# Optimization experiments

Hardware: AMD Instinct MI355X
Metric: run time of the kernel (lower is better)

## Reference

```python
import jax, jax.numpy as jnp
import numpy as np

C = 256          # hidden_size
H = 8            # num_heads
HD = C // H      # head dim = 32
W = 8            # window side; N = W*W = 64 tokens per window
N = W * W
NW = 64          # windows per image
B = 32           # images
B_ = B * NW      # 2048


def make_rel_index():
    # identical to the torch buffer construction (meshgrid 'ij')
    coords = np.stack(np.meshgrid(np.arange(W), np.arange(W), indexing='ij'))  # (2,W,W)
    flat = coords.reshape(2, -1)                       # (2, N)
    rel = flat[:, :, None] - flat[:, None, :]          # (2, N, N)
    rel = rel.transpose(1, 2, 0).astype(np.int64)      # (N, N, 2)
    rel[..., 0] += W - 1
    rel[..., 1] += W - 1
    rel[..., 0] *= 2 * W - 1
    return jnp.asarray(rel.sum(-1), jnp.int32)         # (N, N) in [0, 225)


def setup_inputs() -> dict:
    key = jax.random.key(0)
    ks = jax.random.split(key, 12)
    x = jax.random.normal(ks[0], (B_, N, C), jnp.float32)
    # Swin-style additive mask: 0 for allowed, -1e9 for masked pairs
    keep = jax.random.uniform(ks[1], (NW, N, N)) > 0.1
    mask = jnp.where(keep, 0.0, -1e9).astype(jnp.float32)
    std = 0.02
    wq = jax.random.normal(ks[2], (C, C), jnp.float32) * std
    bq = jnp.zeros((C,), jnp.float32)
    wk = jax.random.normal(ks[3], (C, C), jnp.float32) * std
    bk = jnp.zeros((C,), jnp.float32)
    wv = jax.random.normal(ks[4], (C, C), jnp.float32) * std
    bv = jnp.zeros((C,), jnp.float32)
    wp = jax.random.normal(ks[5], (C, C), jnp.float32) * std
    bp = jnp.zeros((C,), jnp.float32)
    bias_table = jax.random.normal(ks[6], ((2 * W - 1) ** 2, H), jnp.float32) * std
    rel_index = make_rel_index()
    return {"x": x, "mask": mask, "wq": wq, "bq": bq, "wk": wk, "bk": bk,
            "wv": wv, "bv": bv, "wp": wp, "bp": bp,
            "bias_table": bias_table, "rel_index": rel_index}


def reference(x, mask, wq, bq, wk, bk, wv, bv, wp, bp, bias_table, rel_index):
    B_, N, C = x.shape
    nW = mask.shape[0]
    H = bias_table.shape[1]
    HD = C // H
    scale = HD ** -0.5

    def heads(t):  # (B_, N, C) -> (B_, H, N, HD)
        return t.reshape(B_, N, H, HD).transpose(0, 2, 1, 3)

    q = heads(x @ wq + bq) * scale
    k = heads(x @ wk + bk)
    v = heads(x @ wv + bv)

    attn = jnp.einsum('bhnd,bhmd->bhnm', q, k)            # (B_, H, N, N)
    bias = bias_table[rel_index]                          # (N, N, H)
    attn = attn + bias.transpose(2, 0, 1)[None]           # + (1, H, N, N)
    # add per-window shift mask, broadcast over batch and heads
    attn = attn.reshape(B_ // nW, nW, H, N, N) + mask[None, :, None]
    attn = jax.nn.softmax(attn.reshape(B_, H, N, N), axis=-1)

    out = jnp.einsum('bhnm,bhmd->bhnd', attn, v)          # (B_, H, N, HD)
    out = out.transpose(0, 2, 1, 3).reshape(B_, N, C)
    return out @ wp + bp
```

## Files before the change

### kernel.cpp

```cpp
#include <hip/hip_runtime.h>
#include <hip/hip_bf16.h>

typedef __bf16 bf16;
typedef __bf16 bf16x4 __attribute__((ext_vector_type(4)));
typedef __bf16 bf16x8 __attribute__((ext_vector_type(8)));
typedef float  f32x4  __attribute__((ext_vector_type(4)));
typedef short  s16x4  __attribute__((ext_vector_type(4)));

#define DEVI __device__ __forceinline__

static constexpr float kScale = 0.17677669529663687f;

DEVI f32x4 mfma32(bf16x8 a, bf16x8 b, f32x4 c) {
  return __builtin_amdgcn_mfma_f32_16x16x32_bf16(a, b, c, 0, 0, 0);
}
DEVI f32x4 mfma16(bf16x4 a, bf16x4 b, f32x4 c) {
#if __has_builtin(__builtin_amdgcn_mfma_f32_16x16x16bf16_1k)
  return __builtin_amdgcn_mfma_f32_16x16x16bf16_1k(
      __builtin_bit_cast(s16x4, a), __builtin_bit_cast(s16x4, b), c, 0, 0, 0);
#else
  f32x4 d;
  asm volatile("v_mfma_f32_16x16x16_bf16 %0, %1, %2, %3"
               : "=v"(d)
               : "v"(a), "v"(b), "v"(c));
  return d;
#endif
}
DEVI bf16x4 pk4(f32x4 v) {
  bf16x4 p;
  p[0] = (bf16)v[0]; p[1] = (bf16)v[1]; p[2] = (bf16)v[2]; p[3] = (bf16)v[3];
  return p;
}

__global__ __launch_bounds__(256) void prep_kernel(
    const float* __restrict__ wq, const float* __restrict__ bq,
    const float* __restrict__ wk, const float* __restrict__ bk,
    const float* __restrict__ wv, const float* __restrict__ bv,
    const float* __restrict__ wp,
    const float* __restrict__ bias_table, const int* __restrict__ rel_index,
    const float* __restrict__ mask,
    char* __restrict__ wstream, char* __restrict__ wpstream,
    float* __restrict__ bqkv, float* __restrict__ biasM) {
  int idx = blockIdx.x * 256 + threadIdx.x;
  if (idx < 196608) {
    int m = idx >> 16, n = idx & 255, k = (idx >> 8) & 255;
    const float* w = (m == 0) ? wq : (m == 1 ? wk : wv);
    float v = w[k * 256 + n];
    if (m == 0) v *= kScale;
    *(bf16*)(wstream + (size_t)(m * 4 + (k >> 6)) * 32768 + n * 128 +
             (((k & 63) * 2) ^ ((n & 7) << 4))) = (bf16)v;
  } else if (idx < 262144) {
    int rem = idx - 196608;
    int n = rem & 255, k = (rem >> 8) & 255;
    *(bf16*)(wpstream + (size_t)(k >> 6) * 32768 + n * 128 +
             (((k & 63) * 2) ^ ((n & 7) << 4))) = (bf16)wp[k * 256 + n];
  } else if (idx < 262912) {
    int rem = idx - 262144;
    int m = rem >> 8, n = rem & 255;
    const float* b = (m == 0) ? bq : (m == 1 ? bk : bv);
    float v = b[n];
    if (m == 0) v *= kScale;
    bqkv[rem] = v;
  } else if (idx < 2360064) {
    int rem = idx - 262912;
    int w = rem >> 15, h = (rem >> 12) & 7, ij = rem & 4095;
    biasM[rem] = bias_table[rel_index[ij] * 8 + h] + mask[w * 4096 + ij];
  }
}

__global__ __launch_bounds__(256, 2) void swin_kernel(
    const float* __restrict__ x, const char* __restrict__ wstream,
    const char* __restrict__ wpstream, const float* __restrict__ bqkv,
    const float* __restrict__ bp, const float* __restrict__ biasM,
    float* __restrict__ out) {
  __shared__ __align__(16) char xs_ob[32768];
  __shared__ __align__(16) char wbuf[32768];

  int tid = threadIdx.x;
  int w = tid >> 6, lane = tid & 63;
  int g = lane >> 4, c = lane & 15;
  int win = blockIdx.x;
  const f32x4 fz = {0.f, 0.f, 0.f, 0.f};

  {
    const char* xw = (const char*)(x + (size_t)win * 16384);
#pragma unroll
    for (int i = 0; i < 8; ++i) {
      int gb = i * 8192 + tid * 32;
      float4 f0 = *(const float4*)(xw + gb);
      float4 f1 = *(const float4*)(xw + gb + 16);
      bf16x8 v;
      v[0] = (bf16)f0.x; v[1] = (bf16)f0.y; v[2] = (bf16)f0.z; v[3] = (bf16)f0.w;
      v[4] = (bf16)f1.x; v[5] = (bf16)f1.y; v[6] = (bf16)f1.z; v[7] = (bf16)f1.w;
      int t = gb >> 10, ir = (gb & 1023) >> 1;
      *(bf16x8*)(xs_ob + ((t * 512 + ir) ^ ((t & 7) << 4))) = v;
    }
  }
  bf16x8 gr[8];
#pragma unroll
  for (int i = 0; i < 8; ++i)
    gr[i] = *(const bf16x8*)(wstream + (size_t)i * 4096 + (size_t)tid * 16);

  bf16x4 qp[4][4], kp[4][4], vp[4][4];
  f32x4 acc[4][4];

  for (int cc = 0; cc < 12; ++cc) {
    int m = cc >> 2, kq = cc & 3;
    __syncthreads();
#pragma unroll
    for (int i = 0; i < 8; ++i)
      *(bf16x8*)(wbuf + i * 4096 + tid * 16) = gr[i];
    if (cc < 11) {
      size_t base = (size_t)(cc + 1) * 32768;
#pragma unroll
      for (int i = 0; i < 8; ++i)
        gr[i] = *(const bf16x8*)(wstream + base + (size_t)i * 4096 + (size_t)tid * 16);
    } else {
#pragma unroll
      for (int i = 0; i < 8; ++i)
        gr[i] = *(const bf16x8*)(wpstream + (size_t)i * 4096 + (size_t)tid * 16);
    }
    __syncthreads();

    if (kq == 0) {
      if (m < 2) {
#pragma unroll
        for (int nt = 0; nt < 4; ++nt) {
          f32x4 b4 = *(const f32x4*)(bqkv + m * 256 + w * 64 + nt * 16 + g * 4);
#pragma unroll
          for (int tt = 0; tt < 4; ++tt) acc[tt][nt] = b4;
        }
      } else {
#pragma unroll
        for (int nt = 0; nt < 4; ++nt) {
          float bv_ = bqkv[512 + w * 64 + nt * 16 + c];
          f32x4 b4 = {bv_, bv_, bv_, bv_};
#pragma unroll
          for (int tt = 0; tt < 4; ++tt) acc[tt][nt] = b4;
        }
      }
    }
#pragma unroll
    for (int kb = 0; kb < 2; ++kb) {
      bf16x8 xf[4], wf[4];
#pragma unroll
      for (int tt = 0; tt < 4; ++tt)
        xf[tt] = *(const bf16x8*)(
            xs_ob + (((tt * 16 + c) * 512 + (kq * 64 + kb * 32 + g * 8) * 2) ^ ((c & 7) << 4)));
#pragma unroll
      for (int nt = 0; nt < 4; ++nt)
        wf[nt] = *(const bf16x8*)(
            wbuf + (w * 64 + nt * 16 + c) * 128 + ((kb * 64 + g * 16) ^ ((c & 7) << 4)));
      if (m < 2) {
#pragma unroll
        for (int tt = 0; tt < 4; ++tt)
#pragma unroll
          for (int nt = 0; nt < 4; ++nt)
            acc[tt][nt] = mfma32(wf[nt], xf[tt], acc[tt][nt]);
      } else {
#pragma unroll
        for (int tt = 0; tt < 4; ++tt)
#pragma unroll
          for (int nt = 0; nt < 4; ++nt)
            acc[tt][nt] = mfma32(xf[tt], wf[nt], acc[tt][nt]);
      }
    }
    if (kq == 3) {
#pragma unroll
      for (int tt = 0; tt < 4; ++tt)
#pragma unroll
        for (int nt = 0; nt < 4; ++nt) {
          if (m == 0)      qp[tt][nt] = pk4(acc[tt][nt]);
          else if (m == 1) kp[tt][nt] = pk4(acc[tt][nt]);
          else             vp[tt][nt] = pk4(acc[tt][nt]);
        }
    }
  }
  __syncthreads();

#pragma unroll
  for (int hh = 0; hh < 2; ++hh) {
    int h = w * 2 + hh;
    const float* bm = biasM + ((size_t)(win & 63) * 8 + h) * 4096;
#pragma unroll
    for (int mi = 0; mi < 4; ++mi) {
      f32x4 s[4];
#pragma unroll
      for (int mj = 0; mj < 4; ++mj)
        s[mj] = *(const f32x4*)(bm + (mi * 16 + c) * 64 + mj * 16 + g * 4);
#pragma unroll
      for (int dd = 0; dd < 2; ++dd)
#pragma unroll
        for (int mj = 0; mj < 4; ++mj)
          s[mj] = mfma16(kp[mj][hh * 2 + dd], qp[mi][hh * 2 + dd], s[mj]);
      float mx;
      {
        f32x4 m4 = s[0];
#pragma unroll
        for (int mj = 1; mj < 4; ++mj) {
          m4[0] = fmaxf(m4[0], s[mj][0]); m4[1] = fmaxf(m4[1], s[mj][1]);
          m4[2] = fmaxf(m4[2], s[mj][2]); m4[3] = fmaxf(m4[3], s[mj][3]);
        }
        mx = fmaxf(fmaxf(m4[0], m4[1]), fmaxf(m4[2], m4[3]));
        mx = fmaxf(mx, __shfl_xor(mx, 16));
        mx = fmaxf(mx, __shfl_xor(mx, 32));
      }
      float sum;
      {
        f32x4 s4 = fz;
#pragma unroll
        for (int mj = 0; mj < 4; ++mj) {
#pragma unroll
          for (int r = 0; r < 4; ++r) s[mj][r] = __expf(s[mj][r] - mx);
          s4 += s[mj];
        }
        sum = (s4[0] + s4[1]) + (s4[2] + s4[3]);
        sum += __shfl_xor(sum, 16);
        sum += __shfl_xor(sum, 32);
      }
      float rs = 1.0f / sum;
      bf16x4 pf[4];
#pragma unroll
      for (int mj = 0; mj < 4; ++mj) pf[mj] = pk4(s[mj]);
#pragma unroll
      for (int dt = 0; dt < 2; ++dt) {
        f32x4 o = fz;
#pragma unroll
        for (int mj = 0; mj < 4; ++mj)
          o = mfma16(vp[mj][hh * 2 + dt], pf[mj], o);
        bf16x4 ov;
        ov[0] = (bf16)(o[0] * rs); ov[1] = (bf16)(o[1] * rs);
        ov[2] = (bf16)(o[2] * rs); ov[3] = (bf16)(o[3] * rs);
        *(bf16x4*)(xs_ob + (((mi * 16 + c) * 512 + (h * 32 + dt * 16 + g * 4) * 2) ^
                            ((c & 7) << 4))) = ov;
      }
    }
  }

  f32x4 acc2[4][4];
#pragma unroll
  for (int nt = 0; nt < 4; ++nt) {
    f32x4 b4 = *(const f32x4*)(bp + w * 64 + nt * 16 + g * 4);
#pragma unroll
    for (int tt = 0; tt < 4; ++tt) acc2[tt][nt] = b4;
  }
  for (int cc = 0; cc < 4; ++cc) {
    __syncthreads();
#pragma unroll
    for (int i = 0; i < 8; ++i)
      *(bf16x8*)(wbuf + i * 4096 + tid * 16) = gr[i];
    if (cc < 3) {
      size_t base = (size_t)(cc + 1) * 32768;
#pragma unroll
      for (int i = 0; i < 8; ++i)
        gr[i] = *(const bf16x8*)(wpstream + base + (size_t)i * 4096 + (size_t)tid * 16);
    }
    __syncthreads();
#pragma unroll
    for (int kb = 0; kb < 2; ++kb) {
      bf16x8 of[4], wf[4];
#pragma unroll
      for (int tt = 0; tt < 4; ++tt)
        of[tt] = *(const bf16x8*)(
            xs_ob + (((tt * 16 + c) * 512 + (cc * 64 + kb * 32 + g * 8) * 2) ^ ((c & 7) << 4)));
#pragma unroll
      for (int nt = 0; nt < 4; ++nt)
        wf[nt] = *(const bf16x8*)(
            wbuf + (w * 64 + nt * 16 + c) * 128 + ((kb * 64 + g * 16) ^ ((c & 7) << 4)));
#pragma unroll
      for (int tt = 0; tt < 4; ++tt)
#pragma unroll
        for (int nt = 0; nt < 4; ++nt)
          acc2[tt][nt] = mfma32(wf[nt], of[tt], acc2[tt][nt]);
    }
  }
#pragma unroll
  for (int tt = 0; tt < 4; ++tt)
#pragma unroll
    for (int nt = 0; nt < 4; ++nt)
      *(f32x4*)(out + ((size_t)win * 64 + tt * 16 + c) * 256 + w * 64 + nt * 16 + g * 4) =
          acc2[tt][nt];
}

extern "C" void kernel_launch(void* const* d_in, const int* in_sizes, int n_in,
                              void* d_out, int out_size, void* d_ws, size_t ws_size,
                              hipStream_t stream) {
  const float* x          = (const float*)d_in[0];
  const float* mask       = (const float*)d_in[1];
  const float* wq         = (const float*)d_in[2];
  const float* bq         = (const float*)d_in[3];
  const float* wk         = (const float*)d_in[4];
  const float* bk         = (const float*)d_in[5];
  const float* wv         = (const float*)d_in[6];
  const float* bv         = (const float*)d_in[7];
  const float* wp         = (const float*)d_in[8];
  const float* bp         = (const float*)d_in[9];
  const float* bias_table = (const float*)d_in[10];
  const int*   rel_index  = (const int*)d_in[11];

  char* ws = (char*)d_ws;
  size_t o = 0;
  char* wstream = ws + o;  o += (size_t)12 * 32768;
  char* wpstream = ws + o; o += (size_t)4 * 32768;
  float* bqkv = (float*)(ws + o); o += (size_t)768 * 4;
  float* biasM = (float*)(ws + o); o += (size_t)64 * 8 * 64 * 64 * 4;
  if (ws_size < o) return;

  prep_kernel<<<9219, 256, 0, stream>>>(wq, bq, wk, bk, wv, bv, wp,
                                        bias_table, rel_index, mask,
                                        wstream, wpstream, bqkv, biasM);
  swin_kernel<<<2048, 256, 0, stream>>>(x, wstream, wpstream, bqkv, bp, biasM,
                                        (float*)d_out);
}
```

Measured before the change: 160.9 us.

## Double-buffer weight chunks in LDS with single barrier per step and remap windows

Splits the streamed weight chunks into 16KB K=32 slices held in two LDS buffers, so the next slice is written while the current one is consumed, cutting barriers from two per chunk to one. The prep kernel relayouts the weight streams with a matching 64-byte row swizzle. It also permutes the block-to-window mapping so that consecutively scheduled blocks hit different mask windows, which may change L2 locality of biasM. The cost is more loop iterations, each with fewer MFMAs, plus a possible change in LDS bank-conflict behaviour from the new swizzle.

```diff
diff --git a/kernel.cpp b/kernel.cpp
--- a/kernel.cpp
+++ b/kernel.cpp
@@ -47,13 +47,13 @@
     const float* w = (m == 0) ? wq : (m == 1 ? wk : wv);
     float v = w[k * 256 + n];
     if (m == 0) v *= kScale;
-    *(bf16*)(wstream + (size_t)(m * 4 + (k >> 6)) * 32768 + n * 128 +
-             (((k & 63) * 2) ^ ((n & 7) << 4))) = (bf16)v;
+    *(bf16*)(wstream + (size_t)(m * 8 + (k >> 5)) * 16384 + n * 64 +
+             (((k & 31) * 2) ^ ((n & 3) << 4))) = (bf16)v;
   } else if (idx < 262144) {
     int rem = idx - 196608;
     int n = rem & 255, k = (rem >> 8) & 255;
-    *(bf16*)(wpstream + (size_t)(k >> 6) * 32768 + n * 128 +
-             (((k & 63) * 2) ^ ((n & 7) << 4))) = (bf16)wp[k * 256 + n];
+    *(bf16*)(wpstream + (size_t)(k >> 5) * 16384 + n * 64 +
+             (((k & 31) * 2) ^ ((n & 3) << 4))) = (bf16)wp[k * 256 + n];
   } else if (idx < 262912) {
     int rem = idx - 262144;
     int m = rem >> 8, n = rem & 255;
@@ -79,7 +79,8 @@
   int tid = threadIdx.x;
   int w = tid >> 6, lane = tid & 63;
   int g = lane >> 4, c = lane & 15;
-  int win = blockIdx.x;
+  int bid = blockIdx.x;
+  int win = (bid & 7) * 256 + ((bid >> 3) & 3) * 64 + (bid >> 5);
   const f32x4 fz = {0.f, 0.f, 0.f, 0.f};
 
   {
@@ -96,31 +97,46 @@
       *(bf16x8*)(xs_ob + ((t * 512 + ir) ^ ((t & 7) << 4))) = v;
     }
   }
-  bf16x8 gr[8];
-#pragma unroll
-  for (int i = 0; i < 8; ++i)
-    gr[i] = *(const bf16x8*)(wstream + (size_t)i * 4096 + (size_t)tid * 16);
+  bf16x8 gr[4];
+#pragma unroll
+  for (int j = 0; j < 4; ++j)
+    gr[j] = *(const bf16x8*)(wstream + (size_t)j * 4096 + (size_t)tid * 16);
+#pragma unroll
+  for (int j = 0; j < 4; ++j)
+    *(bf16x8*)(wbuf + j * 4096 + tid * 16) = gr[j];
+#pragma unroll
+  for (int j = 0; j < 4; ++j)
+    gr[j] = *(const bf16x8*)(wstream + 16384 + (size_t)j * 4096 + (size_t)tid * 16);
+  __syncthreads();
 
   bf16x4 qp[4][4], kp[4][4], vp[4][4];
   f32x4 acc[4][4];
 
-  for (int cc = 0; cc < 12; ++cc) {
-    int m = cc >> 2, kq = cc & 3;
-    __syncthreads();
-#pragma unroll
-    for (int i = 0; i < 8; ++i)
-      *(bf16x8*)(wbuf + i * 4096 + tid * 16) = gr[i];
-    if (cc < 11) {
-      size_t base = (size_t)(cc + 1) * 32768;
-#pragma unroll
-      for (int i = 0; i < 8; ++i)
-        gr[i] = *(const bf16x8*)(wstream + base + (size_t)i * 4096 + (size_t)tid * 16);
-    } else {
-#pragma unroll
-      for (int i = 0; i < 8; ++i)
-        gr[i] = *(const bf16x8*)(wpstream + (size_t)i * 4096 + (size_t)tid * 16);
-    }
-    __syncthreads();
+  for (int i = 0; i < 24; ++i) {
+    int m = i >> 3, kq = i & 7;
+    char* cur = wbuf + (i & 1) * 16384;
+    char* nxt = wbuf + ((i + 1) & 1) * 16384;
+
+    bf16x8 xf[4], wf[4];
+#pragma unroll
+    for (int tt = 0; tt < 4; ++tt)
+      xf[tt] = *(const bf16x8*)(
+          xs_ob + (((tt * 16 + c) * 512 + kq * 64 + g * 16) ^ ((c & 7) << 4)));
+#pragma unroll
+    for (int nt = 0; nt < 4; ++nt)
+      wf[nt] = *(const bf16x8*)(
+          cur + (w * 64 + nt * 16 + c) * 64 + ((g * 16) ^ ((c & 3) << 4)));
+
+#pragma unroll
+    for (int j = 0; j < 4; ++j)
+      *(bf16x8*)(nxt + j * 4096 + tid * 16) = gr[j];
+    {
+      const char* src = (i < 22) ? (wstream + (size_t)(i + 2) * 16384)
+                                 : (wpstream + (size_t)(i - 22) * 16384);
+#pragma unroll
+      for (int j = 0; j < 4; ++j)
+        gr[j] = *(const bf16x8*)(src + (size_t)j * 4096 + (size_t)tid * 16);
+    }
 
     if (kq == 0) {
       if (m < 2) {
@@ -140,32 +156,20 @@
         }
       }
     }
-#pragma unroll
-    for (int kb = 0; kb < 2; ++kb) {
-      bf16x8 xf[4], wf[4];
+    if (m < 2) {
 #pragma unroll
       for (int tt = 0; tt < 4; ++tt)
-        xf[tt] = *(const bf16x8*)(
-            xs_ob + (((tt * 16 + c) * 512 + (kq * 64 + kb * 32 + g * 8) * 2) ^ ((c & 7) << 4)));
-#pragma unroll
-      for (int nt = 0; nt < 4; ++nt)
-        wf[nt] = *(const bf16x8*)(
-            wbuf + (w * 64 + nt * 16 + c) * 128 + ((kb * 64 + g * 16) ^ ((c & 7) << 4)));
-      if (m < 2) {
-#pragma unroll
-        for (int tt = 0; tt < 4; ++tt)
-#pragma unroll
-          for (int nt = 0; nt < 4; ++nt)
-            acc[tt][nt] = mfma32(wf[nt], xf[tt], acc[tt][nt]);
-      } else {
-#pragma unroll
-        for (int tt = 0; tt < 4; ++tt)
-#pragma unroll
-          for (int nt = 0; nt < 4; ++nt)
-            acc[tt][nt] = mfma32(xf[tt], wf[nt], acc[tt][nt]);
-      }
-    }
-    if (kq == 3) {
+#pragma unroll
+        for (int nt = 0; nt < 4; ++nt)
+          acc[tt][nt] = mfma32(wf[nt], xf[tt], acc[tt][nt]);
+    } else {
+#pragma unroll
+      for (int tt = 0; tt < 4; ++tt)
+#pragma unroll
+        for (int nt = 0; nt < 4; ++nt)
+          acc[tt][nt] = mfma32(xf[tt], wf[nt], acc[tt][nt]);
+    }
+    if (kq == 7) {
 #pragma unroll
       for (int tt = 0; tt < 4; ++tt)
 #pragma unroll
@@ -175,8 +179,8 @@
           else             vp[tt][nt] = pk4(acc[tt][nt]);
         }
     }
-  }
-  __syncthreads();
+    __syncthreads();
+  }
 
 #pragma unroll
   for (int hh = 0; hh < 2; ++hh) {
@@ -236,6 +240,7 @@
       }
     }
   }
+  __syncthreads();
 
   f32x4 acc2[4][4];
 #pragma unroll
@@ -244,35 +249,38 @@
 #pragma unroll
     for (int tt = 0; tt < 4; ++tt) acc2[tt][nt] = b4;
   }
-  for (int cc = 0; cc < 4; ++cc) {
-    __syncthreads();
-#pragma unroll
-    for (int i = 0; i < 8; ++i)
-      *(bf16x8*)(wbuf + i * 4096 + tid * 16) = gr[i];
-    if (cc < 3) {
-      size_t base = (size_t)(cc + 1) * 32768;
-#pragma unroll
-      for (int i = 0; i < 8; ++i)
-        gr[i] = *(const bf16x8*)(wpstream + base + (size_t)i * 4096 + (size_t)tid * 16);
-    }
-    __syncthreads();
-#pragma unroll
-    for (int kb = 0; kb < 2; ++kb) {
-      bf16x8 of[4], wf[4];
-#pragma unroll
-      for (int tt = 0; tt < 4; ++tt)
-        of[tt] = *(const bf16x8*)(
-            xs_ob + (((tt * 16 + c) * 512 + (cc * 64 + kb * 32 + g * 8) * 2) ^ ((c & 7) << 4)));
+  for (int i = 24; i < 32; ++i) {
+    int cc = i - 24;
+    char* cur = wbuf + (i & 1) * 16384;
+    char* nxt = wbuf + ((i + 1) & 1) * 16384;
+
+    bf16x8 of[4], wf[4];
+#pragma unroll
+    for (int tt = 0; tt < 4; ++tt)
+      of[tt] = *(const bf16x8*)(
+          xs_ob + (((tt * 16 + c) * 512 + cc * 64 + g * 16) ^ ((c & 7) << 4)));
+#pragma unroll
+    for (int nt = 0; nt < 4; ++nt)
+      wf[nt] = *(const bf16x8*)(
+          cur + (w * 64 + nt * 16 + c) * 64 + ((g * 16) ^ ((c & 3) << 4)));
+
+    if (i <= 30) {
+#pragma unroll
+      for (int j = 0; j < 4; ++j)
+        *(bf16x8*)(nxt + j * 4096 + tid * 16) = gr[j];
+      if (i <= 29) {
+#pragma unroll
+        for (int j = 0; j < 4; ++j)
+          gr[j] = *(const bf16x8*)(wpstream + (size_t)(i - 22) * 16384 +
+                                   (size_t)j * 4096 + (size_t)tid * 16);
+      }
+    }
+#pragma unroll
+    for (int tt = 0; tt < 4; ++tt)
 #pragma unroll
       for (int nt = 0; nt < 4; ++nt)
-        wf[nt] = *(const bf16x8*)(
-            wbuf + (w * 64 + nt * 16 + c) * 128 + ((kb * 64 + g * 16) ^ ((c & 7) << 4)));
-#pragma unroll
-      for (int tt = 0; tt < 4; ++tt)
-#pragma unroll
-        for (int nt = 0; nt < 4; ++nt)
-          acc2[tt][nt] = mfma32(wf[nt], of[tt], acc2[tt][nt]);
-    }
+        acc2[tt][nt] = mfma32(wf[nt], of[tt], acc2[tt][nt]);
+    if (i < 31) __syncthreads();
   }
 #pragma unroll
   for (int tt = 0; tt < 4; ++tt)
@@ -300,8 +308,8 @@
 
   char* ws = (char*)d_ws;
   size_t o = 0;
-  char* wstream = ws + o;  o += (size_t)12 * 32768;
-  char* wpstream = ws + o; o += (size_t)4 * 32768;
+  char* wstream = ws + o;  o += (size_t)24 * 16384;
+  char* wpstream = ws + o; o += (size_t)8 * 16384;
   float* bqkv = (float*)(ws + o); o += (size_t)768 * 4;
   float* biasM = (float*)(ws + o); o += (size_t)64 * 8 * 64 * 64 * 4;
   if (ws_size < o) return;
```

New measurement: 165.5 us. 2.9% more time.
